# Optimization experiments

Hardware: AMD Instinct MI355X
Metric: run time of the kernel (lower is better)

## Reference

```python
import jax, jax.numpy as jnp
import numpy as np

B, L, CI, D, H, DFF, MODES, EL, NC, MA = 32, 512, 21, 512, 8, 2048, 32, 3, 10, 25
EH = D // H


def _modes_index(seq_len, modes, seed=0):
    m = min(modes, seq_len // 2)
    idx = np.arange(seq_len // 2)
    np.random.RandomState(seed).shuffle(idx)
    return np.sort(idx[:m])

MODES_IDX = _modes_index(L, MODES)


def _pos_emb(length, d):
    pos = np.arange(length, dtype=np.float32)[:, None]
    div = np.exp(np.arange(0, d, 2, dtype=np.float32) * -(np.log(10000.0) / d))
    pe = np.zeros((length, d), np.float32)
    pe[:, 0::2] = np.sin(pos * div)
    pe[:, 1::2] = np.cos(pos * div)
    return jnp.asarray(pe)


def _decomp_res(x, k=MA):
    # series_decomp: x - moving_average(x), edge-replicated padding, stride 1
    p = (k - 1) // 2
    xp = jnp.concatenate([jnp.repeat(x[:, :1], p, axis=1), x, jnp.repeat(x[:, -1:], p, axis=1)], axis=1)
    cs = jnp.cumsum(xp, axis=1)
    cs = jnp.concatenate([jnp.zeros_like(cs[:, :1]), cs], axis=1)
    ma = (cs[:, k:] - cs[:, :-k]) / k  # [B, L, D]
    return x - ma


def _forward(x_enc, token_w, Wq, bq, Wk, bk, Wv, bv, Wo, bo, fwr, fwi, conv1_w, conv2_w, ln_w, ln_b, proj_w, proj_b):
    b, l, _ = x_enc.shape
    # TokenEmbedding: Conv1d(k=3, padding=1, circular, no bias)
    xp = jnp.concatenate([x_enc[:, -1:], x_enc, x_enc[:, :1]], axis=1)
    x = jax.lax.conv_general_dilated(xp, token_w, (1,), 'VALID', dimension_numbers=('NWC', 'WIO', 'NWC'))
    x = x + _pos_emb(l, D)[None]
    idx = MODES_IDX
    m = idx.shape[0]
    nf = l // 2 + 1
    for li in range(EL):
        # AutoCorrelationLayer projections (k/v computed but unused by FourierBlock)
        q = (x @ Wq[li] + bq[li]).reshape(b, l, H, EH)
        _ = x @ Wk[li] + bk[li]
        _ = x @ Wv[li] + bv[li]
        xh = jnp.transpose(q, (0, 2, 3, 1))            # [B,H,E,L]
        x_ft = jnp.fft.rfft(xh, axis=-1)               # [B,H,E,L//2+1]
        xg = x_ft[..., idx]                            # gather selected modes [B,H,E,M]
        w = fwr[li] + 1j * fwi[li]                     # [H,E,E,M] complex
        og = jnp.einsum('bhem,heom->bhom', xg, w)      # per-mode complex matmul
        # torch places result at ordinal position wi (not i): dense prefix, zeros after
        out_ft = jnp.concatenate([og, jnp.zeros((b, H, EH, nf - m), og.dtype)], axis=-1)
        o = jnp.fft.irfft(out_ft, n=l, axis=-1)        # [B,H,E,L] real
        # faithful to torch's out.view(B, L, -1) on contiguous [B,H,E,L]
        new_x = o.reshape(b, l, H * EH) @ Wo[li] + bo[li]
        x = _decomp_res(x + new_x)
        y = jax.nn.gelu(x @ conv1_w[li], approximate=False) @ conv2_w[li]
        x = _decomp_res(x + y)
    # my_Layernorm: LayerNorm then subtract per-batch temporal mean
    mu = jnp.mean(x, -1, keepdims=True)
    var = jnp.mean((x - mu) ** 2, -1, keepdims=True)
    xh2 = (x - mu) / jnp.sqrt(var + 1e-5) * ln_w + ln_b
    x = xh2 - jnp.mean(xh2, axis=1, keepdims=True)
    out = jax.nn.gelu(x, approximate=False)
    return out.reshape(b, -1) @ proj_w + proj_b


def setup_inputs() -> dict:
    key = jax.random.key(0)
    ks = jax.random.split(key, 16)
    s = 0.02
    return {
        'x_enc': jax.random.normal(ks[0], (B, L, CI), jnp.float32),
        'token_w': jax.random.normal(ks[1], (3, CI, D), jnp.float32) * (2.0 / (3 * CI)) ** 0.5,
        'Wq': jax.random.normal(ks[2], (EL, D, D), jnp.float32) * D ** -0.5,
        'bq': jnp.zeros((EL, D), jnp.float32),
        'Wk': jax.random.normal(ks[3], (EL, D, D), jnp.float32) * D ** -0.5,
        'bk': jnp.zeros((EL, D), jnp.float32),
        'Wv': jax.random.normal(ks[4], (EL, D, D), jnp.float32) * D ** -0.5,
        'bv': jnp.zeros((EL, D), jnp.float32),
        'Wo': jax.random.normal(ks[5], (EL, D, D), jnp.float32) * D ** -0.5,
        'bo': jnp.zeros((EL, D), jnp.float32),
        'fwr': jax.random.uniform(ks[6], (EL, H, EH, EH, MODES), jnp.float32) * s,
        'fwi': jax.random.uniform(ks[7], (EL, H, EH, EH, MODES), jnp.float32) * s,
        'conv1_w': jax.random.normal(ks[8], (EL, D, DFF), jnp.float32) * D ** -0.5,
        'conv2_w': jax.random.normal(ks[9], (EL, DFF, D), jnp.float32) * DFF ** -0.5,
        'ln_w': jnp.ones((D,), jnp.float32),
        'ln_b': jnp.zeros((D,), jnp.float32),
        'proj_w': jax.random.normal(ks[10], (L * D, NC), jnp.float32) * (L * D) ** -0.5,
        'proj_b': jnp.zeros((NC,), jnp.float32),
    }


def reference(x_enc, token_w, Wq, bq, Wk, bk, Wv, bv, Wo, bo, fwr, fwi, conv1_w, conv2_w, ln_w, ln_b, proj_w, proj_b):
    return _forward(x_enc, token_w, Wq, bq, Wk, bk, Wv, bv, Wo, bo, fwr, fwi, conv1_w, conv2_w, ln_w, ln_b, proj_w, proj_b)
```

## Files before the change

kernel.cpp:

```cpp
#include <hip/hip_runtime.h>
#include <hip/hip_bf16.h>
#include <stdint.h>
#include <algorithm>

#define BB  32
#define LL  512
#define NCI 21
#define DD  512
#define NH  8
#define EHH 64
#define NDFF 2048
#define NM  32
#define NEL 3
#define NCC 10

struct Modes { int v[NM]; };

typedef __bf16 bf16x8 __attribute__((ext_vector_type(8)));
typedef float f32x4 __attribute__((ext_vector_type(4)));

__device__ __forceinline__ float erf_poly(float x) {
    float ax = fabsf(x);
    float t = 1.0f / fmaf(0.3275911f, ax, 1.0f);
    float y = t * fmaf(t, fmaf(t, fmaf(t, fmaf(t, 1.061405429f, -1.453152027f),
                                       1.421413741f), -0.284496736f), 0.254829592f);
    float r = 1.0f - y * __expf(-ax * ax);
    return copysignf(r, x);
}

__device__ __forceinline__ float gelu_f(float x) {
    return 0.5f * x * (1.0f + erf_poly(x * 0.7071067811865475f));
}

__device__ __forceinline__ void gload_lds16(const void* g, void* l) {
    __builtin_amdgcn_global_load_lds((const __attribute__((address_space(1))) void*)g,
                                     (__attribute__((address_space(3))) void*)l, 16, 0, 0);
}

__global__ void k_pegen(float* __restrict__ PE) {
    int l = blockIdx.x;
    for (int d = threadIdx.x; d < DD; d += 256) {
        int a = d & ~1;
        float freq = expf((float)a * (-9.210340371976184f / 512.0f));
        float v = (float)l * freq;
        PE[l * DD + d] = (d & 1) ? cosf(v) : sinf(v);
    }
}

__global__ __launch_bounds__(256) void k_embed(const float* __restrict__ xe,
        const float* __restrict__ tw, const float* __restrict__ PE,
        __hip_bfloat16* __restrict__ Xb) {
    int lc = blockIdx.x, dh = blockIdx.y, b = blockIdx.z;
    int t = threadIdx.x;
    int d = dh * 256 + t;
    __shared__ float s_xe[34][NCI];
    int l0 = lc * 32;
    for (int i = t; i < 34 * NCI; i += 256) {
        int r = i / NCI, c = i % NCI;
        int ls = (l0 - 1 + r + LL) & (LL - 1);
        s_xe[r][c] = xe[(b * LL + ls) * NCI + c];
    }
    float twr[63];
    #pragma unroll
    for (int kc = 0; kc < 63; ++kc) twr[kc] = tw[kc * DD + d];
    __syncthreads();
    for (int li = 0; li < 32; ++li) {
        int l = l0 + li;
        float acc = 0.f;
        #pragma unroll
        for (int k = 0; k < 3; ++k)
            #pragma unroll
            for (int c = 0; c < NCI; ++c)
                acc = fmaf(s_xe[li + k][c], twr[k * NCI + c], acc);
        float r = acc + PE[l * DD + d];
        Xb[((size_t)(b * LL + l)) * DD + d] = __float2bfloat16(r);
    }
}

__global__ void k_wt(const float* __restrict__ W, __hip_bfloat16* __restrict__ WT,
                     int K, int N) {
    __shared__ float s[32][33];
    int bx = blockIdx.x;
    int by = blockIdx.y;
    int t = threadIdx.x;
    int r = t >> 5, c = t & 31;
    #pragma unroll
    for (int i = 0; i < 4; ++i)
        s[r + i * 8][c] = W[(size_t)(by * 32 + r + i * 8) * N + bx * 32 + c];
    __syncthreads();
    #pragma unroll
    for (int i = 0; i < 4; ++i) {
        int n = bx * 32 + r + i * 8;
        WT[(size_t)n * K + by * 32 + c] = __float2bfloat16(s[c][r + i * 8]);
    }
}

__global__ void k_wfm(const float* __restrict__ fwr, const float* __restrict__ fwi,
                      float2* __restrict__ WM, int li) {
    int blk = blockIdx.x;
    int h = blk >> 6, e = blk & 63;
    int t = threadIdx.x;
    __shared__ float2 s[32][65];
    const float* br = fwr + (((size_t)(li * NH + h) * EHH + e) * EHH) * NM;
    const float* bi = fwi + (((size_t)(li * NH + h) * EHH + e) * EHH) * NM;
    for (int i = t; i < 2048; i += 256) {
        int o = i >> 5, m = i & 31;
        s[m][o] = make_float2(br[i], bi[i]);
    }
    __syncthreads();
    int mr = t >> 6, o = t & 63;
    for (int m = mr; m < 32; m += 4)
        WM[((size_t)(h * 32 + m)) * 4096 + e * 64 + o] = s[m][o];
}

__global__ void k_tgen(__hip_bfloat16* __restrict__ Tb, Modes md) {
    int r = blockIdx.x;
    int m = r >> 1;
    int im = md.v[m];
    const float w0 = 6.283185307179586f / 512.0f;
    for (int l = threadIdx.x; l < LL; l += 64) {
        int red = (im * l) & 511;
        float ang = w0 * (float)red;
        float v = (r & 1) ? sinf(ang) : cosf(ang);
        Tb[r * 512 + l] = __float2bfloat16(v);
    }
}

__global__ void k_sgen(__hip_bfloat16* __restrict__ Sk) {
    int k = blockIdx.x;
    int m = k >> 1;
    const float w0 = 6.283185307179586f / 512.0f;
    for (int l = threadIdx.x; l < LL; l += 64) {
        int red = (m * l) & 511;
        float ang = w0 * (float)red;
        float v;
        if ((k & 1) == 0) v = cosf(ang) * (m == 0 ? (1.0f / 512.0f) : (2.0f / 512.0f));
        else              v = -sinf(ang) * (2.0f / 512.0f);
        Sk[k * 512 + l] = __float2bfloat16(v);
    }
}

__global__ __launch_bounds__(256) void k_xt(const __hip_bfloat16* __restrict__ Xb,
                                            __hip_bfloat16* __restrict__ XT) {
    int b = blockIdx.z;
    int l0 = blockIdx.x * 64, d0 = blockIdx.y * 64;
    __shared__ float s[64][65];
    const __hip_bfloat16* xb = Xb + (size_t)b * LL * DD;
    int t = threadIdx.x;
    #pragma unroll
    for (int i = 0; i < 16; ++i) {
        int e = i * 256 + t;
        int lr = e >> 6, dc = e & 63;
        s[lr][dc] = __bfloat162float(xb[(size_t)(l0 + lr) * DD + d0 + dc]);
    }
    __syncthreads();
    __hip_bfloat16* xt = XT + (size_t)b * DD * LL;
    #pragma unroll
    for (int i = 0; i < 16; ++i) {
        int e = i * 256 + t;
        int dr = e >> 6, lc = e & 63;
        xt[(size_t)(d0 + dr) * LL + l0 + lc] = __float2bfloat16(s[lc][dr]);
    }
}

__global__ __launch_bounds__(256) void k_tx(const __hip_bfloat16* __restrict__ Tb,
        const __hip_bfloat16* __restrict__ XT, __hip_bfloat16* __restrict__ TX) {
    __shared__ __hip_bfloat16 Ts[64 * 32];
    __shared__ __hip_bfloat16 Xs[128 * 32];
    int b = blockIdx.x, n0 = blockIdx.y * 128;
    int t = threadIdx.x, w = t >> 6, ln = t & 63;
    const __hip_bfloat16* xb = XT + (size_t)b * DD * LL;
    f32x4 acc[4][2] = {};
    for (int k0 = 0; k0 < 512; k0 += 32) {
        {
            int row = w * 16 + (ln >> 2), q = ln & 3;
            gload_lds16(Tb + row * 512 + k0 + q * 8, (char*)Ts + w * 1024);
        }
        #pragma unroll
        for (int i = 0; i < 2; ++i) {
            int s = i * 256 + t;
            int row = s >> 2, q = s & 3;
            gload_lds16(xb + (size_t)(n0 + row) * LL + k0 + q * 8,
                        (char*)Xs + i * 4096 + w * 1024);
        }
        __syncthreads();
        int lr = ln & 15, kc = (ln >> 4) * 8;
        bf16x8 af[4], bfr[2];
        #pragma unroll
        for (int mi = 0; mi < 4; ++mi)
            af[mi] = *(const bf16x8*)&Ts[(mi * 16 + lr) * 32 + kc];
        #pragma unroll
        for (int ni = 0; ni < 2; ++ni)
            bfr[ni] = *(const bf16x8*)&Xs[(w * 32 + ni * 16 + lr) * 32 + kc];
        #pragma unroll
        for (int mi = 0; mi < 4; ++mi)
            #pragma unroll
            for (int ni = 0; ni < 2; ++ni)
                acc[mi][ni] = __builtin_amdgcn_mfma_f32_16x16x32_bf16(
                    af[mi], bfr[ni], acc[mi][ni], 0, 0, 0);
        __syncthreads();
    }
    int rb = (ln >> 4) * 4, cb = ln & 15;
    #pragma unroll
    for (int mi = 0; mi < 4; ++mi)
        #pragma unroll
        for (int ni = 0; ni < 2; ++ni)
            #pragma unroll
            for (int j = 0; j < 4; ++j) {
                int m = mi * 16 + rb + j;
                int col = n0 + w * 32 + ni * 16 + cb;
                TX[(size_t)(b * 64 + m) * 512 + col] =
                    __float2bfloat16(acc[mi][ni][j]);
            }
}

__global__ __launch_bounds__(256) void k_swt(const __hip_bfloat16* __restrict__ Sk,
        const __hip_bfloat16* __restrict__ WT, __hip_bfloat16* __restrict__ SWT) {
    __shared__ __hip_bfloat16 Ts[64 * 32];
    __shared__ __hip_bfloat16 Xs[128 * 32];
    int n0 = blockIdx.x * 128;
    int t = threadIdx.x, w = t >> 6, ln = t & 63;
    f32x4 acc[4][2] = {};
    for (int k0 = 0; k0 < 512; k0 += 32) {
        {
            int row = w * 16 + (ln >> 2), q = ln & 3;
            gload_lds16(Sk + row * 512 + k0 + q * 8, (char*)Ts + w * 1024);
        }
        #pragma unroll
        for (int i = 0; i < 2; ++i) {
            int s = i * 256 + t;
            int row = s >> 2, q = s & 3;
            gload_lds16(WT + (size_t)(n0 + row) * 512 + k0 + q * 8,
                        (char*)Xs + i * 4096 + w * 1024);
        }
        __syncthreads();
        int lr = ln & 15, kc = (ln >> 4) * 8;
        bf16x8 af[4], bfr[2];
        #pragma unroll
        for (int mi = 0; mi < 4; ++mi)
            af[mi] = *(const bf16x8*)&Ts[(mi * 16 + lr) * 32 + kc];
        #pragma unroll
        for (int ni = 0; ni < 2; ++ni)
            bfr[ni] = *(const bf16x8*)&Xs[(w * 32 + ni * 16 + lr) * 32 + kc];
        #pragma unroll
        for (int mi = 0; mi < 4; ++mi)
            #pragma unroll
            for (int ni = 0; ni < 2; ++ni)
                acc[mi][ni] = __builtin_amdgcn_mfma_f32_16x16x32_bf16(
                    af[mi], bfr[ni], acc[mi][ni], 0, 0, 0);
        __syncthreads();
    }
    int rb = (ln >> 4) * 4, cb = ln & 15;
    #pragma unroll
    for (int mi = 0; mi < 4; ++mi)
        #pragma unroll
        for (int ni = 0; ni < 2; ++ni)
            #pragma unroll
            for (int j = 0; j < 4; ++j) {
                int k = mi * 16 + rb + j;
                int col = n0 + w * 32 + ni * 16 + cb;
                SWT[(size_t)col * 64 + k] = __float2bfloat16(acc[mi][ni][j]);
            }
}

__global__ __launch_bounds__(256) void k_xg(const __hip_bfloat16* __restrict__ A,
        const __hip_bfloat16* __restrict__ Bt, const float* __restrict__ bq,
        float* __restrict__ XGr, float* __restrict__ XGi, Modes md) {
    __shared__ __hip_bfloat16 As[128 * 32];
    __shared__ __hip_bfloat16 Bs[128 * 32];
    int t = threadIdx.x;
    int m0 = blockIdx.x * 128, n0 = blockIdx.y * 128;
    int w = t >> 6, ln = t & 63;
    int wr = w >> 1, wc = w & 1;
    const int K = 512;
    f32x4 acc[4][4] = {};
    for (int k0 = 0; k0 < K; k0 += 32) {
        #pragma unroll
        for (int i = 0; i < 2; ++i) {
            int s = i * 256 + t;
            int row = s >> 2, q = s & 3;
            gload_lds16(A + (size_t)(m0 + row) * K + k0 + q * 8,
                        (char*)As + i * 4096 + w * 1024);
            gload_lds16(Bt + (size_t)(n0 + row) * K + k0 + q * 8,
                        (char*)Bs + i * 4096 + w * 1024);
        }
        __syncthreads();
        bf16x8 af[4], bfr[4];
        int lr = ln & 15, kc = (ln >> 4) * 8;
        #pragma unroll
        for (int mi = 0; mi < 4; ++mi)
            af[mi] = *(const bf16x8*)&As[(wr * 64 + mi * 16 + lr) * 32 + kc];
        #pragma unroll
        for (int ni = 0; ni < 4; ++ni)
            bfr[ni] = *(const bf16x8*)&Bs[(wc * 64 + ni * 16 + lr) * 32 + kc];
        #pragma unroll
        for (int mi = 0; mi < 4; ++mi)
            #pragma unroll
            for (int ni = 0; ni < 4; ++ni)
                acc[mi][ni] = __builtin_amdgcn_mfma_f32_16x16x32_bf16(
                    af[mi], bfr[ni], acc[mi][ni], 0, 0, 0);
        __syncthreads();
    }
    int rb = (ln >> 4) * 4, cb = ln & 15;
    #pragma unroll
    for (int mi = 0; mi < 4; ++mi) {
        #pragma unroll
        for (int ni = 0; ni < 4; ++ni) {
            int col = n0 + wc * 64 + ni * 16 + cb;
            int h = col >> 6, e = col & 63;
            #pragma unroll
            for (int j = 0; j < 4; ++j) {
                int row = m0 + wr * 64 + mi * 16 + rb + j;
                int b = row >> 6, r = row & 63, m = r >> 1;
                float v = acc[mi][ni][j];
                int off = (h * 32 + m) * 2048 + e * 32 + b;
                if ((r & 1) == 0)
                    XGr[off] = v + (md.v[m] == 0 ? 512.f * bq[col] : 0.f);
                else
                    XGi[off] = -v;
            }
        }
    }
}

template<int EPI>
__global__ __launch_bounds__(256, 3) void k_ffn(const __hip_bfloat16* __restrict__ A,
        const __hip_bfloat16* __restrict__ Bt, __hip_bfloat16* __restrict__ Cb,
        int M, int N, int K) {
    constexpr int TILE = 256 * 32;
    __shared__ __hip_bfloat16 lds[3 * TILE];
    int t = threadIdx.x, w = t >> 6, ln = t & 63;
    int wr = w >> 1, wc = w & 1;
    int lr = ln & 15, q16 = ln >> 4;
    int m0 = blockIdx.x * 128, n0 = blockIdx.y * 128;
    f32x4 acc[4][4] = {};
    int NT = K / 32;

    auto STAGE = [&](int buf, int kt) {
        int kb = kt * 32;
        char* ldsA = (char*)(lds + buf * TILE);
        char* ldsB = ldsA + 128 * 64;
        #pragma unroll
        for (int i = 0; i < 2; ++i) {
            int c = i * 256 + t;
            int row = c >> 2, q = c & 3;
            int slot = q ^ ((row >> 1) & 3);
            gload_lds16(A + (size_t)(m0 + row) * K + kb + slot * 8,
                        ldsA + (i * 256 + w * 64) * 16);
        }
        #pragma unroll
        for (int i = 0; i < 2; ++i) {
            int c = i * 256 + t;
            int row = c >> 2, q = c & 3;
            int slot = q ^ ((row >> 1) & 3);
            gload_lds16(Bt + (size_t)(n0 + row) * K + kb + slot * 8,
                        ldsB + (i * 256 + w * 64) * 16);
        }
    };

    STAGE(0, 0);
    STAGE(1, 1);
    for (int kt = 0; kt < NT; ++kt) {
        if (kt + 1 < NT) asm volatile("s_waitcnt vmcnt(4)" ::: "memory");
        else             asm volatile("s_waitcnt vmcnt(0)" ::: "memory");
        __builtin_amdgcn_sched_barrier(0);
        __builtin_amdgcn_s_barrier();
        __builtin_amdgcn_sched_barrier(0);
        if (kt + 2 < NT) STAGE((kt + 2) % 3, kt + 2);
        const __hip_bfloat16* As = lds + (kt % 3) * TILE;
        const __hip_bfloat16* Bs = As + 128 * 32;
        bf16x8 a[4], b[4];
        #pragma unroll
        for (int mi = 0; mi < 4; ++mi) {
            int row = wr * 64 + mi * 16 + lr;
            int s = q16 ^ ((row >> 1) & 3);
            a[mi] = *(const bf16x8*)&As[row * 32 + s * 8];
        }
        #pragma unroll
        for (int ni = 0; ni < 4; ++ni) {
            int row = wc * 64 + ni * 16 + lr;
            int s = q16 ^ ((row >> 1) & 3);
            b[ni] = *(const bf16x8*)&Bs[row * 32 + s * 8];
        }
        __builtin_amdgcn_s_setprio(1);
        #pragma unroll
        for (int mi = 0; mi < 4; ++mi)
            #pragma unroll
            for (int ni = 0; ni < 4; ++ni)
                acc[mi][ni] = __builtin_amdgcn_mfma_f32_16x16x32_bf16(
                    a[mi], b[ni], acc[mi][ni], 0, 0, 0);
        __builtin_amdgcn_s_setprio(0);
    }
    int rb = q16 * 4;
    #pragma unroll
    for (int mi = 0; mi < 4; ++mi) {
        #pragma unroll
        for (int ni = 0; ni < 4; ++ni) {
            int col = n0 + wc * 64 + ni * 16 + lr;
            int rowb = m0 + wr * 64 + mi * 16 + rb;
            #pragma unroll
            for (int j = 0; j < 4; ++j) {
                float v = acc[mi][ni][j];
                size_t off = (size_t)(rowb + j) * N + col;
                if (EPI == 1) Cb[off] = __float2bfloat16(gelu_f(v));
                else Cb[off] = __float2bfloat16(v);
            }
        }
    }
}

__global__ __launch_bounds__(256) void k_og(const float* __restrict__ XGr,
        const float* __restrict__ XGi, const float2* __restrict__ WM,
        __hip_bfloat16* __restrict__ OGT) {
    int hm = blockIdx.x;
    int t = threadIdx.x;
    __shared__ float2 sw[4096];
    __shared__ float sxr[2048], sxi[2048];
    const float2* w = WM + (size_t)hm * 4096;
    for (int i = t; i < 4096; i += 256) sw[i] = w[i];
    const float* xr = XGr + hm * 2048;
    const float* xi = XGi + hm * 2048;
    for (int i = t; i < 2048; i += 256) { sxr[i] = xr[i]; sxi[i] = xi[i]; }
    __syncthreads();
    int b = t >> 3, o0 = (t & 7) * 8;
    float ar[8] = {}, ai[8] = {};
    for (int e = 0; e < 64; ++e) {
        float xrv = sxr[e * 32 + b], xiv = sxi[e * 32 + b];
        #pragma unroll
        for (int j = 0; j < 8; ++j) {
            float2 wv = sw[e * 64 + o0 + j];
            ar[j] = fmaf(xrv, wv.x, fmaf(-xiv, wv.y, ar[j]));
            ai[j] = fmaf(xrv, wv.y, fmaf( xiv, wv.x, ai[j]));
        }
    }
    int h = hm >> 5, m = hm & 31;
    __hip_bfloat16* og = OGT + (size_t)b * (512 * 64);
    #pragma unroll
    for (int j = 0; j < 8; ++j) {
        int he = h * 64 + o0 + j;
        union { __hip_bfloat16 h2[2]; uint32_t u; } pk;
        pk.h2[0] = __float2bfloat16(ar[j]);
        pk.h2[1] = __float2bfloat16(ai[j]);
        *(uint32_t*)&og[he * 64 + 2 * m] = pk.u;
    }
}

__global__ __launch_bounds__(256) void k_nx(const __hip_bfloat16* __restrict__ OGT,
        const __hip_bfloat16* __restrict__ SWT, const float* __restrict__ bo,
        __hip_bfloat16* __restrict__ Cb) {
    __shared__ __hip_bfloat16 As[128 * 32];
    __shared__ __hip_bfloat16 Bs[128 * 32];
    int t = threadIdx.x;
    int m0 = blockIdx.x * 128, n0 = blockIdx.y * 128, b = blockIdx.z;
    int w = t >> 6, ln = t & 63;
    int wr = w >> 1, wc = w & 1;
    const __hip_bfloat16* ab = OGT + (size_t)b * 512 * 64;
    f32x4 acc[4][4] = {};
    for (int k0 = 0; k0 < 64; k0 += 32) {
        #pragma unroll
        for (int i = 0; i < 2; ++i) {
            int s = i * 256 + t;
            int row = s >> 2, q = s & 3;
            gload_lds16(ab + (size_t)(m0 + row) * 64 + k0 + q * 8,
                        (char*)As + i * 4096 + w * 1024);
            gload_lds16(SWT + (size_t)(n0 + row) * 64 + k0 + q * 8,
                        (char*)Bs + i * 4096 + w * 1024);
        }
        __syncthreads();
        bf16x8 af[4], bfr[4];
        int lr = ln & 15, kc = (ln >> 4) * 8;
        #pragma unroll
        for (int mi = 0; mi < 4; ++mi)
            af[mi] = *(const bf16x8*)&As[(wr * 64 + mi * 16 + lr) * 32 + kc];
        #pragma unroll
        for (int ni = 0; ni < 4; ++ni)
            bfr[ni] = *(const bf16x8*)&Bs[(wc * 64 + ni * 16 + lr) * 32 + kc];
        #pragma unroll
        for (int mi = 0; mi < 4; ++mi)
            #pragma unroll
            for (int ni = 0; ni < 4; ++ni)
                acc[mi][ni] = __builtin_amdgcn_mfma_f32_16x16x32_bf16(
                    af[mi], bfr[ni], acc[mi][ni], 0, 0, 0);
        __syncthreads();
    }
    int rb = (ln >> 4) * 4, cb = ln & 15;
    #pragma unroll
    for (int mi = 0; mi < 4; ++mi) {
        #pragma unroll
        for (int ni = 0; ni < 4; ++ni) {
            int col = n0 + wc * 64 + ni * 16 + cb;
            int he = m0 + wr * 64 + mi * 16 + rb;
            float bv = bo[col];
            #pragma unroll
            for (int j = 0; j < 4; ++j)
                Cb[((size_t)b * 512 + he + j) * 512 + col] =
                    __float2bfloat16(acc[mi][ni][j] + bv);
        }
    }
}

__global__ void k_add_decomp(const __hip_bfloat16* __restrict__ P,
                             const __hip_bfloat16* __restrict__ Q,
                             __hip_bfloat16* __restrict__ Outb) {
    int b = blockIdx.x >> 3;
    int l0 = (blockIdx.x & 7) * 64;
    int d = threadIdx.x;
    const __hip_bfloat16* p = P + (size_t)b * LL * DD + d;
    const __hip_bfloat16* q = Q + (size_t)b * LL * DD + d;
    __hip_bfloat16* ob = Outb + (size_t)b * LL * DD + d;
    float sum = 0.f;
    for (int j = l0 - 12; j <= l0 + 12; ++j) {
        int jc = j < 0 ? 0 : (j > 511 ? 511 : j);
        sum += __bfloat162float(p[jc * DD]) + __bfloat162float(q[jc * DD]);
    }
    for (int l = l0; l < l0 + 64; ++l) {
        float sv = __bfloat162float(p[l * DD]) + __bfloat162float(q[l * DD]);
        float r = sv - sum * (1.0f / 25.0f);
        ob[l * DD] = __float2bfloat16(r);
        int lp = l + 13 > 511 ? 511 : l + 13;
        int lm = l - 12 < 0 ? 0 : l - 12;
        sum += (__bfloat162float(p[lp * DD]) + __bfloat162float(q[lp * DD]))
             - (__bfloat162float(p[lm * DD]) + __bfloat162float(q[lm * DD]));
    }
}

__global__ void k_ln(const __hip_bfloat16* __restrict__ Xin, const float* __restrict__ lw,
                     const float* __restrict__ lb, float* __restrict__ Out) {
    int row = blockIdx.x;
    int t = threadIdx.x;
    bf16x8 xv = *(const bf16x8*)(Xin + (size_t)row * DD + t * 8);
    float x[8];
    #pragma unroll
    for (int j = 0; j < 8; ++j) x[j] = (float)xv[j];
    float s = 0.f;
    #pragma unroll
    for (int j = 0; j < 8; ++j) s += x[j];
    #pragma unroll
    for (int o = 32; o; o >>= 1) s += __shfl_down(s, o);
    float mu = __shfl(s, 0) * (1.0f / 512.0f);
    float vs = 0.f;
    #pragma unroll
    for (int j = 0; j < 8; ++j) { x[j] -= mu; vs += x[j] * x[j]; }
    #pragma unroll
    for (int o = 32; o; o >>= 1) vs += __shfl_down(vs, o);
    float var = __shfl(vs, 0) * (1.0f / 512.0f);
    float rstd = rsqrtf(var + 1e-5f);
    float4 w0 = ((const float4*)lw)[t * 2], w1 = ((const float4*)lw)[t * 2 + 1];
    float4 b0 = ((const float4*)lb)[t * 2], b1 = ((const float4*)lb)[t * 2 + 1];
    float4 r0, r1;
    r0.x = x[0] * rstd * w0.x + b0.x; r0.y = x[1] * rstd * w0.y + b0.y;
    r0.z = x[2] * rstd * w0.z + b0.z; r0.w = x[3] * rstd * w0.w + b0.w;
    r1.x = x[4] * rstd * w1.x + b1.x; r1.y = x[5] * rstd * w1.y + b1.y;
    r1.z = x[6] * rstd * w1.z + b1.z; r1.w = x[7] * rstd * w1.w + b1.w;
    float4* o4 = (float4*)(Out + (size_t)row * DD);
    o4[t * 2] = r0; o4[t * 2 + 1] = r1;
}

__global__ void k_colmean(const float* __restrict__ A, float* __restrict__ CM) {
    int col0 = blockIdx.x * 64;
    int part = threadIdx.x >> 6;
    int cl = threadIdx.x & 63;
    int col = col0 + cl;
    int b = col >> 9, d = col & 511;
    const float* a = A + (size_t)b * LL * DD + d;
    float s = 0.f;
    for (int l = part * 128; l < part * 128 + 128; ++l) s += a[l * DD];
    __shared__ float red[4][64];
    red[part][cl] = s;
    __syncthreads();
    if (threadIdx.x < 64) {
        float v = red[0][cl] + red[1][cl] + red[2][cl] + red[3][cl];
        CM[col0 + cl] = v * (1.0f / 512.0f);
    }
}

__global__ __launch_bounds__(256) void k_proj_partial(const float* __restrict__ A,
        const float* __restrict__ CM, const float* __restrict__ PW,
        float* __restrict__ PP) {
    int b = blockIdx.x, c = blockIdx.y;
    int t = threadIdx.x;
    float acc[NCC] = {};
    const float* a = A + (size_t)b * LL * DD;
    const float* cm = CM + (b << 9);
    int i0 = c * 16384, i1 = i0 + 16384;
    for (int i = i0 + t; i < i1; i += 256) {
        float v = gelu_f(a[i] - cm[i & 511]);
        const float* w = PW + (size_t)i * NCC;
        #pragma unroll
        for (int n = 0; n < NCC; ++n) acc[n] = fmaf(v, w[n], acc[n]);
    }
    __shared__ float red[4][NCC];
    int lane = t & 63, wv = t >> 6;
    #pragma unroll
    for (int n = 0; n < NCC; ++n) {
        float s = acc[n];
        #pragma unroll
        for (int o = 32; o; o >>= 1) s += __shfl_down(s, o);
        if (lane == 0) red[wv][n] = s;
    }
    __syncthreads();
    if (t < NCC) {
        PP[(b * 16 + c) * NCC + t] = red[0][t] + red[1][t] + red[2][t] + red[3][t];
    }
}

__global__ void k_proj_final(const float* __restrict__ PP, const float* __restrict__ pb,
                             float* __restrict__ out) {
    int t = threadIdx.x;
    if (t >= BB * NCC) return;
    int b = t / NCC, n = t % NCC;
    float s = pb[n];
    for (int c = 0; c < 16; ++c) s += PP[(b * 16 + c) * NCC + n];
    out[t] = s;
}

static void compute_modes(int* out) {
    static uint32_t mt[624];
    uint32_t s = 0u;
    mt[0] = s;
    for (int i = 1; i < 624; ++i)
        mt[i] = 1812433253u * (mt[i - 1] ^ (mt[i - 1] >> 30)) + (uint32_t)i;
    int mti = 624;
    auto genrand = [&]() -> uint32_t {
        if (mti >= 624) {
            for (int k = 0; k < 624; ++k) {
                uint32_t y = (mt[k] & 0x80000000u) | (mt[(k + 1) % 624] & 0x7fffffffu);
                mt[k] = mt[(k + 397) % 624] ^ (y >> 1) ^ ((y & 1u) ? 2567483615u : 0u);
            }
            mti = 0;
        }
        uint32_t y = mt[mti++];
        y ^= y >> 11;
        y ^= (y << 7) & 2636928640u;
        y ^= (y << 15) & 4022730752u;
        y ^= y >> 18;
        return y;
    };
    int idx[256];
    for (int i = 0; i < 256; ++i) idx[i] = i;
    for (int i = 255; i >= 1; --i) {
        uint32_t mx = (uint32_t)i;
        uint32_t mask = mx;
        mask |= mask >> 1; mask |= mask >> 2; mask |= mask >> 4;
        mask |= mask >> 8; mask |= mask >> 16;
        uint32_t j;
        while ((j = (genrand() & mask)) > mx) {}
        int tmp = idx[i]; idx[i] = idx[j]; idx[j] = tmp;
    }
    int sel[NM];
    for (int i = 0; i < NM; ++i) sel[i] = idx[i];
    std::sort(sel, sel + NM);
    for (int i = 0; i < NM; ++i) out[i] = sel[i];
}

extern "C" void kernel_launch(void* const* d_in, const int* in_sizes, int n_in,
                              void* d_out, int out_size, void* d_ws, size_t ws_size,
                              hipStream_t stream) {
    const float* xe  = (const float*)d_in[0];
    const float* tw  = (const float*)d_in[1];
    const float* Wq  = (const float*)d_in[2];
    const float* bq  = (const float*)d_in[3];
    const float* Wo  = (const float*)d_in[8];
    const float* bo  = (const float*)d_in[9];
    const float* fwr = (const float*)d_in[10];
    const float* fwi = (const float*)d_in[11];
    const float* W1  = (const float*)d_in[12];
    const float* W2  = (const float*)d_in[13];
    const float* lw  = (const float*)d_in[14];
    const float* lb  = (const float*)d_in[15];
    const float* pw  = (const float*)d_in[16];
    const float* pb  = (const float*)d_in[17];
    float* out = (float*)d_out;

    const size_t NX = (size_t)BB * LL * DD;
    const size_t NHF = (size_t)BB * LL * NDFF;
    const size_t NXG = (size_t)BB * NH * EHH * NM;
    const size_t NWM = (size_t)NH * NM * EHH * EHH;

    char* wsb = (char*)d_ws;
    size_t off = 0;
    float* TB  = (float*)(wsb + off); off += NX * 4;
    float* XGr = (float*)(wsb + off); off += NXG * 4;
    float* XGi = (float*)(wsb + off); off += NXG * 4;
    __hip_bfloat16* X1b = (__hip_bfloat16*)(wsb + off); off += NX * 2;
    __hip_bfloat16* X2b = (__hip_bfloat16*)(wsb + off); off += NX * 2;
    __hip_bfloat16* HMb = (__hip_bfloat16*)(wsb + off); off += NHF * 2;
    __hip_bfloat16* WT  = (__hip_bfloat16*)(wsb + off); off += (size_t)DD * DD * 2;
    float2* WM          = (float2*)(wsb + off);         off += NWM * 8;
    __hip_bfloat16* TXb = (__hip_bfloat16*)(wsb + off); off += (size_t)BB * 64 * 512 * 2;
    __hip_bfloat16* Tb  = (__hip_bfloat16*)(wsb + off); off += (size_t)64 * 512 * 2;
    __hip_bfloat16* OGT = (__hip_bfloat16*)(wsb + off); off += (size_t)BB * 512 * 64 * 2;
    __hip_bfloat16* Sk  = (__hip_bfloat16*)(wsb + off); off += (size_t)64 * 512 * 2;
    __hip_bfloat16* WTq = (__hip_bfloat16*)(wsb + off); off += (size_t)NEL * DD * DD * 2;
    __hip_bfloat16* WT1 = (__hip_bfloat16*)(wsb + off); off += (size_t)NEL * DD * NDFF * 2;
    __hip_bfloat16* WT2 = (__hip_bfloat16*)(wsb + off); off += (size_t)NEL * NDFF * DD * 2;
    __hip_bfloat16* SW3 = (__hip_bfloat16*)(wsb + off); off += (size_t)NEL * DD * 64 * 2;
    float* PE           = (float*)(wsb + off);          off += (size_t)LL * DD * 4;
    if (ws_size < off) return;

    __hip_bfloat16* XTb = (__hip_bfloat16*)TB;
    __hip_bfloat16* TBb = (__hip_bfloat16*)((char*)TB + NX * 2);

    Modes mi;
    compute_modes(mi.v);

    k_pegen<<<512, 256, 0, stream>>>(PE);
    k_embed<<<dim3(16, 2, BB), 256, 0, stream>>>(xe, tw, PE, X1b);
    k_tgen<<<64, 64, 0, stream>>>(Tb, mi);
    k_sgen<<<64, 64, 0, stream>>>(Sk);
    for (int li = 0; li < NEL; ++li) {
        k_wt<<<dim3(16, 16), 256, 0, stream>>>(Wq + (size_t)li * DD * DD,
                                               WTq + (size_t)li * DD * DD, DD, DD);
        k_wt<<<dim3(64, 16), 256, 0, stream>>>(W1 + (size_t)li * DD * NDFF,
                                               WT1 + (size_t)li * DD * NDFF, DD, NDFF);
        k_wt<<<dim3(16, 64), 256, 0, stream>>>(W2 + (size_t)li * NDFF * DD,
                                               WT2 + (size_t)li * NDFF * DD, NDFF, DD);
        k_wt<<<dim3(16, 16), 256, 0, stream>>>(Wo + (size_t)li * DD * DD, WT, DD, DD);
        k_swt<<<4, 256, 0, stream>>>(Sk, WT, SW3 + (size_t)li * DD * 64);
    }

    __hip_bfloat16* curb = X1b;
    __hip_bfloat16* altb = X2b;
    const int M = BB * LL;

    for (int li = 0; li < NEL; ++li) {
        k_wfm<<<NH * EHH, 256, 0, stream>>>(fwr, fwi, WM, li);
        k_xt<<<dim3(8, 8, BB), 256, 0, stream>>>(curb, XTb);
        k_tx<<<dim3(BB, 4), 256, 0, stream>>>(Tb, XTb, TXb);
        k_xg<<<dim3(16, 4), 256, 0, stream>>>(TXb, WTq + (size_t)li * DD * DD,
                                              bq + li * DD, XGr, XGi, mi);
        k_og<<<NH * NM, 256, 0, stream>>>(XGr, XGi, WM, OGT);
        k_nx<<<dim3(4, 4, BB), 256, 0, stream>>>(OGT, SW3 + (size_t)li * DD * 64,
                                                 bo + li * DD, TBb);
        k_add_decomp<<<BB * 8, DD, 0, stream>>>(curb, TBb, altb);
        { __hip_bfloat16* t_ = curb; curb = altb; altb = t_; }
        k_ffn<1><<<dim3(M / 128, NDFF / 128), 256, 0, stream>>>(
            curb, WT1 + (size_t)li * DD * NDFF, HMb, M, NDFF, DD);
        k_ffn<3><<<dim3(M / 128, DD / 128), 256, 0, stream>>>(
            HMb, WT2 + (size_t)li * NDFF * DD, TBb, M, DD, NDFF);
        k_add_decomp<<<BB * 8, DD, 0, stream>>>(curb, TBb, altb);
        { __hip_bfloat16* t_ = curb; curb = altb; altb = t_; }
    }

    k_ln<<<BB * LL, 64, 0, stream>>>(curb, lw, lb, TB);
    float* CM = XGr;
    float* PP = XGi;
    k_colmean<<<256, 256, 0, stream>>>(TB, CM);
    k_proj_partial<<<dim3(BB, 16), 256, 0, stream>>>(TB, CM, pw, PP);
    k_proj_final<<<1, 320, 0, stream>>>(PP, pb, out);
}
```

Baseline: 752.3 us.

## Fuse transposed activation writes into producers and batch setup kernels across layers

```diff
diff --git a/kernel.cpp b/kernel.cpp
--- a/kernel.cpp
+++ b/kernel.cpp
@@ -37,19 +37,41 @@
                                      (__attribute__((address_space(3))) void*)l, 16, 0, 0);
 }
 
-__global__ void k_pegen(float* __restrict__ PE) {
-    int l = blockIdx.x;
-    for (int d = threadIdx.x; d < DD; d += 256) {
-        int a = d & ~1;
-        float freq = expf((float)a * (-9.210340371976184f / 512.0f));
-        float v = (float)l * freq;
-        PE[l * DD + d] = (d & 1) ? cosf(v) : sinf(v);
+__global__ void k_tabs(float* __restrict__ PE, __hip_bfloat16* __restrict__ Tb,
+                       __hip_bfloat16* __restrict__ Sk, Modes md) {
+    int bid = blockIdx.x;
+    const float w0 = 6.283185307179586f / 512.0f;
+    if (bid < 512) {
+        int l = bid;
+        for (int d = threadIdx.x; d < DD; d += 256) {
+            int a = d & ~1;
+            float freq = expf((float)a * (-9.210340371976184f / 512.0f));
+            float v = (float)l * freq;
+            PE[l * DD + d] = (d & 1) ? cosf(v) : sinf(v);
+        }
+    } else if (bid < 576) {
+        int r = bid - 512, m = r >> 1, im = md.v[m];
+        for (int l = threadIdx.x; l < LL; l += 256) {
+            int red = (im * l) & 511;
+            float ang = w0 * (float)red;
+            Tb[r * 512 + l] = __float2bfloat16((r & 1) ? sinf(ang) : cosf(ang));
+        }
+    } else {
+        int k = bid - 576, m = k >> 1;
+        for (int l = threadIdx.x; l < LL; l += 256) {
+            int red = (m * l) & 511;
+            float ang = w0 * (float)red;
+            float v;
+            if ((k & 1) == 0) v = cosf(ang) * (m == 0 ? (1.0f / 512.0f) : (2.0f / 512.0f));
+            else              v = -sinf(ang) * (2.0f / 512.0f);
+            Sk[k * 512 + l] = __float2bfloat16(v);
+        }
     }
 }
 
 __global__ __launch_bounds__(256) void k_embed(const float* __restrict__ xe,
         const float* __restrict__ tw, const float* __restrict__ PE,
-        __hip_bfloat16* __restrict__ Xb) {
+        __hip_bfloat16* __restrict__ Xb, __hip_bfloat16* __restrict__ XT) {
     int lc = blockIdx.x, dh = blockIdx.y, b = blockIdx.z;
     int t = threadIdx.x;
     int d = dh * 256 + t;
@@ -64,21 +86,33 @@
     #pragma unroll
     for (int kc = 0; kc < 63; ++kc) twr[kc] = tw[kc * DD + d];
     __syncthreads();
-    for (int li = 0; li < 32; ++li) {
-        int l = l0 + li;
-        float acc = 0.f;
-        #pragma unroll
-        for (int k = 0; k < 3; ++k)
-            #pragma unroll
-            for (int c = 0; c < NCI; ++c)
-                acc = fmaf(s_xe[li + k][c], twr[k * NCI + c], acc);
-        float r = acc + PE[l * DD + d];
-        Xb[((size_t)(b * LL + l)) * DD + d] = __float2bfloat16(r);
+    __hip_bfloat16* xtp = XT + ((size_t)b * DD + d) * LL + l0;
+    #pragma unroll
+    for (int c8 = 0; c8 < 4; ++c8) {
+        bf16x8 xv;
+        #pragma unroll
+        for (int j = 0; j < 8; ++j) {
+            int li = c8 * 8 + j;
+            int l = l0 + li;
+            float acc = 0.f;
+            #pragma unroll
+            for (int k = 0; k < 3; ++k)
+                #pragma unroll
+                for (int c = 0; c < NCI; ++c)
+                    acc = fmaf(s_xe[li + k][c], twr[k * NCI + c], acc);
+            float r = acc + PE[l * DD + d];
+            __hip_bfloat16 rb = __float2bfloat16(r);
+            Xb[((size_t)(b * LL + l)) * DD + d] = rb;
+            xv[j] = *(__bf16*)&rb;
+        }
+        *(bf16x8*)(xtp + c8 * 8) = xv;
     }
 }
 
 __global__ void k_wt(const float* __restrict__ W, __hip_bfloat16* __restrict__ WT,
                      int K, int N) {
+    size_t loff = (size_t)blockIdx.z * K * N;
+    W += loff; WT += loff;
     __shared__ float s[32][33];
     int bx = blockIdx.x;
     int by = blockIdx.y;
@@ -96,7 +130,8 @@
 }
 
 __global__ void k_wfm(const float* __restrict__ fwr, const float* __restrict__ fwi,
-                      float2* __restrict__ WM, int li) {
+                      float2* __restrict__ WM3) {
+    int li = blockIdx.y;
     int blk = blockIdx.x;
     int h = blk >> 6, e = blk & 63;
     int t = threadIdx.x;
@@ -108,59 +143,10 @@
         s[m][o] = make_float2(br[i], bi[i]);
     }
     __syncthreads();
+    float2* WM = WM3 + (size_t)li * (NH * NM * EHH * EHH);
     int mr = t >> 6, o = t & 63;
     for (int m = mr; m < 32; m += 4)
         WM[((size_t)(h * 32 + m)) * 4096 + e * 64 + o] = s[m][o];
-}
-
-__global__ void k_tgen(__hip_bfloat16* __restrict__ Tb, Modes md) {
-    int r = blockIdx.x;
-    int m = r >> 1;
-    int im = md.v[m];
-    const float w0 = 6.283185307179586f / 512.0f;
-    for (int l = threadIdx.x; l < LL; l += 64) {
-        int red = (im * l) & 511;
-        float ang = w0 * (float)red;
-        float v = (r & 1) ? sinf(ang) : cosf(ang);
-        Tb[r * 512 + l] = __float2bfloat16(v);
-    }
-}
-
-__global__ void k_sgen(__hip_bfloat16* __restrict__ Sk) {
-    int k = blockIdx.x;
-    int m = k >> 1;
-    const float w0 = 6.283185307179586f / 512.0f;
-    for (int l = threadIdx.x; l < LL; l += 64) {
-        int red = (m * l) & 511;
-        float ang = w0 * (float)red;
-        float v;
-        if ((k & 1) == 0) v = cosf(ang) * (m == 0 ? (1.0f / 512.0f) : (2.0f / 512.0f));
-        else              v = -sinf(ang) * (2.0f / 512.0f);
-        Sk[k * 512 + l] = __float2bfloat16(v);
-    }
-}
-
-__global__ __launch_bounds__(256) void k_xt(const __hip_bfloat16* __restrict__ Xb,
-                                            __hip_bfloat16* __restrict__ XT) {
-    int b = blockIdx.z;
-    int l0 = blockIdx.x * 64, d0 = blockIdx.y * 64;
-    __shared__ float s[64][65];
-    const __hip_bfloat16* xb = Xb + (size_t)b * LL * DD;
-    int t = threadIdx.x;
-    #pragma unroll
-    for (int i = 0; i < 16; ++i) {
-        int e = i * 256 + t;
-        int lr = e >> 6, dc = e & 63;
-        s[lr][dc] = __bfloat162float(xb[(size_t)(l0 + lr) * DD + d0 + dc]);
-    }
-    __syncthreads();
-    __hip_bfloat16* xt = XT + (size_t)b * DD * LL;
-    #pragma unroll
-    for (int i = 0; i < 16; ++i) {
-        int e = i * 256 + t;
-        int dr = e >> 6, lc = e & 63;
-        xt[(size_t)(d0 + dr) * LL + l0 + lc] = __float2bfloat16(s[lc][dr]);
-    }
 }
 
 __global__ __launch_bounds__(256) void k_tx(const __hip_bfloat16* __restrict__ Tb,
@@ -215,7 +201,10 @@
 }
 
 __global__ __launch_bounds__(256) void k_swt(const __hip_bfloat16* __restrict__ Sk,
-        const __hip_bfloat16* __restrict__ WT, __hip_bfloat16* __restrict__ SWT) {
+        const __hip_bfloat16* __restrict__ WT3, __hip_bfloat16* __restrict__ SW3) {
+    int li = blockIdx.y;
+    const __hip_bfloat16* WT = WT3 + (size_t)li * DD * DD;
+    __hip_bfloat16* SWT = SW3 + (size_t)li * DD * 64;
     __shared__ __hip_bfloat16 Ts[64 * 32];
     __shared__ __hip_bfloat16 Xs[128 * 32];
     int n0 = blockIdx.x * 128;
@@ -499,28 +488,39 @@
     }
 }
 
+template<bool WRITE_XT>
 __global__ void k_add_decomp(const __hip_bfloat16* __restrict__ P,
                              const __hip_bfloat16* __restrict__ Q,
-                             __hip_bfloat16* __restrict__ Outb) {
+                             __hip_bfloat16* __restrict__ Outb,
+                             __hip_bfloat16* __restrict__ XT) {
     int b = blockIdx.x >> 3;
     int l0 = (blockIdx.x & 7) * 64;
     int d = threadIdx.x;
     const __hip_bfloat16* p = P + (size_t)b * LL * DD + d;
     const __hip_bfloat16* q = Q + (size_t)b * LL * DD + d;
     __hip_bfloat16* ob = Outb + (size_t)b * LL * DD + d;
+    __hip_bfloat16* xtp = WRITE_XT ? (XT + ((size_t)b * DD + d) * LL + l0) : nullptr;
     float sum = 0.f;
     for (int j = l0 - 12; j <= l0 + 12; ++j) {
         int jc = j < 0 ? 0 : (j > 511 ? 511 : j);
         sum += __bfloat162float(p[jc * DD]) + __bfloat162float(q[jc * DD]);
     }
-    for (int l = l0; l < l0 + 64; ++l) {
-        float sv = __bfloat162float(p[l * DD]) + __bfloat162float(q[l * DD]);
-        float r = sv - sum * (1.0f / 25.0f);
-        ob[l * DD] = __float2bfloat16(r);
-        int lp = l + 13 > 511 ? 511 : l + 13;
-        int lm = l - 12 < 0 ? 0 : l - 12;
-        sum += (__bfloat162float(p[lp * DD]) + __bfloat162float(q[lp * DD]))
-             - (__bfloat162float(p[lm * DD]) + __bfloat162float(q[lm * DD]));
+    for (int c8 = 0; c8 < 8; ++c8) {
+        bf16x8 xv;
+        #pragma unroll
+        for (int j8 = 0; j8 < 8; ++j8) {
+            int l = l0 + c8 * 8 + j8;
+            float sv = __bfloat162float(p[l * DD]) + __bfloat162float(q[l * DD]);
+            float r = sv - sum * (1.0f / 25.0f);
+            __hip_bfloat16 rb = __float2bfloat16(r);
+            ob[l * DD] = rb;
+            if (WRITE_XT) xv[j8] = *(__bf16*)&rb;
+            int lp = l + 13 > 511 ? 511 : l + 13;
+            int lm = l - 12 < 0 ? 0 : l - 12;
+            sum += (__bfloat162float(p[lp * DD]) + __bfloat162float(q[lp * DD]))
+                 - (__bfloat162float(p[lm * DD]) + __bfloat162float(q[lm * DD]));
+        }
+        if (WRITE_XT) *(bf16x8*)(xtp + c8 * 8) = xv;
     }
 }
 
@@ -685,8 +685,8 @@
     __hip_bfloat16* X1b = (__hip_bfloat16*)(wsb + off); off += NX * 2;
     __hip_bfloat16* X2b = (__hip_bfloat16*)(wsb + off); off += NX * 2;
     __hip_bfloat16* HMb = (__hip_bfloat16*)(wsb + off); off += NHF * 2;
-    __hip_bfloat16* WT  = (__hip_bfloat16*)(wsb + off); off += (size_t)DD * DD * 2;
-    float2* WM          = (float2*)(wsb + off);         off += NWM * 8;
+    __hip_bfloat16* WT3 = (__hip_bfloat16*)(wsb + off); off += (size_t)NEL * DD * DD * 2;
+    float2* WM3         = (float2*)(wsb + off);         off += (size_t)NEL * NWM * 8;
     __hip_bfloat16* TXb = (__hip_bfloat16*)(wsb + off); off += (size_t)BB * 64 * 512 * 2;
     __hip_bfloat16* Tb  = (__hip_bfloat16*)(wsb + off); off += (size_t)64 * 512 * 2;
     __hip_bfloat16* OGT = (__hip_bfloat16*)(wsb + off); off += (size_t)BB * 512 * 64 * 2;
@@ -704,41 +704,36 @@
     Modes mi;
     compute_modes(mi.v);
 
-    k_pegen<<<512, 256, 0, stream>>>(PE);
-    k_embed<<<dim3(16, 2, BB), 256, 0, stream>>>(xe, tw, PE, X1b);
-    k_tgen<<<64, 64, 0, stream>>>(Tb, mi);
-    k_sgen<<<64, 64, 0, stream>>>(Sk);
-    for (int li = 0; li < NEL; ++li) {
-        k_wt<<<dim3(16, 16), 256, 0, stream>>>(Wq + (size_t)li * DD * DD,
-                                               WTq + (size_t)li * DD * DD, DD, DD);
-        k_wt<<<dim3(64, 16), 256, 0, stream>>>(W1 + (size_t)li * DD * NDFF,
-                                               WT1 + (size_t)li * DD * NDFF, DD, NDFF);
-        k_wt<<<dim3(16, 64), 256, 0, stream>>>(W2 + (size_t)li * NDFF * DD,
-                                               WT2 + (size_t)li * NDFF * DD, NDFF, DD);
-        k_wt<<<dim3(16, 16), 256, 0, stream>>>(Wo + (size_t)li * DD * DD, WT, DD, DD);
-        k_swt<<<4, 256, 0, stream>>>(Sk, WT, SW3 + (size_t)li * DD * 64);
-    }
+    k_tabs<<<640, 256, 0, stream>>>(PE, Tb, Sk, mi);
+    k_embed<<<dim3(16, 2, BB), 256, 0, stream>>>(xe, tw, PE, X1b, XTb);
+    k_wt<<<dim3(16, 16, NEL), 256, 0, stream>>>(Wq, WTq, DD, DD);
+    k_wt<<<dim3(64, 16, NEL), 256, 0, stream>>>(W1, WT1, DD, NDFF);
+    k_wt<<<dim3(16, 64, NEL), 256, 0, stream>>>(W2, WT2, NDFF, DD);
+    k_wt<<<dim3(16, 16, NEL), 256, 0, stream>>>(Wo, WT3, DD, DD);
+    k_swt<<<dim3(4, NEL), 256, 0, stream>>>(Sk, WT3, SW3);
+    k_wfm<<<dim3(NH * EHH, NEL), 256, 0, stream>>>(fwr, fwi, WM3);
 
     __hip_bfloat16* curb = X1b;
     __hip_bfloat16* altb = X2b;
     const int M = BB * LL;
 
     for (int li = 0; li < NEL; ++li) {
-        k_wfm<<<NH * EHH, 256, 0, stream>>>(fwr, fwi, WM, li);
-        k_xt<<<dim3(8, 8, BB), 256, 0, stream>>>(curb, XTb);
         k_tx<<<dim3(BB, 4), 256, 0, stream>>>(Tb, XTb, TXb);
         k_xg<<<dim3(16, 4), 256, 0, stream>>>(TXb, WTq + (size_t)li * DD * DD,
                                               bq + li * DD, XGr, XGi, mi);
-        k_og<<<NH * NM, 256, 0, stream>>>(XGr, XGi, WM, OGT);
+        k_og<<<NH * NM, 256, 0, stream>>>(XGr, XGi, WM3 + (size_t)li * NWM, OGT);
         k_nx<<<dim3(4, 4, BB), 256, 0, stream>>>(OGT, SW3 + (size_t)li * DD * 64,
                                                  bo + li * DD, TBb);
-        k_add_decomp<<<BB * 8, DD, 0, stream>>>(curb, TBb, altb);
+        k_add_decomp<false><<<BB * 8, DD, 0, stream>>>(curb, TBb, altb, nullptr);
         { __hip_bfloat16* t_ = curb; curb = altb; altb = t_; }
         k_ffn<1><<<dim3(M / 128, NDFF / 128), 256, 0, stream>>>(
             curb, WT1 + (size_t)li * DD * NDFF, HMb, M, NDFF, DD);
         k_ffn<3><<<dim3(M / 128, DD / 128), 256, 0, stream>>>(
             HMb, WT2 + (size_t)li * NDFF * DD, TBb, M, DD, NDFF);
-        k_add_decomp<<<BB * 8, DD, 0, stream>>>(curb, TBb, altb);
+        if (li < NEL - 1)
+            k_add_decomp<true><<<BB * 8, DD, 0, stream>>>(curb, TBb, altb, XTb);
+        else
+            k_add_decomp<false><<<BB * 8, DD, 0, stream>>>(curb, TBb, altb, nullptr);
         { __hip_bfloat16* t_ = curb; curb = altb; altb = t_; }
     }
 
```

Result: faster. 718.7 us (-4.5%).
